# Performance work log

Hardware: AMD Instinct MI355X
Metric: run time of the kernel (lower is better)

## Reference

```python
import jax, jax.numpy as jnp
import numpy as np
import math

B, L, D, H, FF = 32, 512, 512, 8, 2048
DH = D // H
EPS = 1e-5

def pe_table(L, D):
    pos = jnp.arange(L, dtype=jnp.float32)[:, None]
    div = jnp.exp(jnp.arange(0, D, 2, dtype=jnp.float32) * (-(math.log(10000.0) / D)))
    pe = jnp.zeros((L, D), dtype=jnp.float32)
    pe = pe.at[:, 0::2].set(jnp.sin(pos * div))
    pe = pe.at[:, 1::2].set(jnp.cos(pos * div))
    return pe

def setup_inputs() -> dict:
    key = jax.random.key(0)
    ks = jax.random.split(key, 16)
    s = 0.02
    inp = {
        "x": jax.random.normal(ks[0], (B, L, D), jnp.float32),
        "mask": jnp.ones((B, L), jnp.int32),
        "speaker_emb": jax.random.normal(ks[1], (B, L, D), jnp.float32),
        "Wg": jax.random.normal(ks[2], (D, D), jnp.float32) * s,
        "Wq": jax.random.normal(ks[3], (D, D), jnp.float32) * s,
        "bq": jnp.zeros((D,), jnp.float32),
        "Wk": jax.random.normal(ks[4], (D, D), jnp.float32) * s,
        "bk": jnp.zeros((D,), jnp.float32),
        "Wv": jax.random.normal(ks[5], (D, D), jnp.float32) * s,
        "bv": jnp.zeros((D,), jnp.float32),
        "Wo": jax.random.normal(ks[6], (D, D), jnp.float32) * s,
        "bo": jnp.zeros((D,), jnp.float32),
        "ln_g": jnp.ones((D,), jnp.float32),
        "ln_b": jnp.zeros((D,), jnp.float32),
        "W1": jax.random.normal(ks[7], (FF, D), jnp.float32) * s,
        "b1": jnp.zeros((FF,), jnp.float32),
        "W2": jax.random.normal(ks[8], (D, FF), jnp.float32) * s,
        "b2": jnp.zeros((D,), jnp.float32),
    }
    return inp

def layer_norm(x, g, b):
    mu = jnp.mean(x, axis=-1, keepdims=True)
    var = jnp.var(x, axis=-1, keepdims=True)
    return (x - mu) * jax.lax.rsqrt(var + EPS) * g + b

def reference(x, mask, speaker_emb, Wg, Wq, bq, Wk, bk, Wv, bv, Wo, bo, ln_g, ln_b, W1, b1, W2, b2):
    # DynamicGating: sigmoid(x W^T) * x
    x = jax.nn.sigmoid(x @ Wg.T) * x
    # speaker embedding + sinusoidal positional encoding (dropout is eval/no-op)
    x = x + speaker_emb + pe_table(L, D)[None, :, :]
    # Multi-head self-attention (eager, full score matrix)
    q = (x @ Wq.T + bq).reshape(B, L, H, DH).transpose(0, 2, 1, 3) / math.sqrt(DH)
    k = (x @ Wk.T + bk).reshape(B, L, H, DH).transpose(0, 2, 1, 3)
    v = (x @ Wv.T + bv).reshape(B, L, H, DH).transpose(0, 2, 1, 3)
    scores = jnp.einsum("bhqd,bhkd->bhqk", q, k)  # (B,H,L,L)
    key_mask = (mask == 0)[:, None, None, :]  # mask keys where mask==0
    scores = jnp.where(key_mask, jnp.float32(-1e10), scores)
    attn = jax.nn.softmax(scores, axis=-1)
    ctx = jnp.einsum("bhqk,bhkd->bhqd", attn, v)
    ctx = ctx.transpose(0, 2, 1, 3).reshape(B, L, D)
    attn_out = ctx @ Wo.T + bo
    h = attn_out + x  # residual (dropout no-op)
    # FeedForwardNet: note GELU applied after BOTH linears (faithful to source)
    mid = jax.nn.gelu(layer_norm(h, ln_g, ln_b) @ W1.T + b1, approximate=True)
    out = jax.nn.gelu(mid @ W2.T + b2, approximate=True)
    return out + h
```

## Files before the change

kernel.cpp:

```cpp
#include <hip/hip_runtime.h>
#include <math.h>

#define Bn 32
#define Ln 512
#define Dn 512
#define Hn 8
#define DHn 64
#define FFn 2048
#define Mn (Bn*Ln)
#define QKVS 1536

typedef __attribute__((ext_vector_type(4))) float f32x4;
typedef __attribute__((ext_vector_type(8))) short short8;

__device__ __forceinline__ float bf2f(ushort u){ return __uint_as_float(((unsigned)u) << 16); }
__device__ __forceinline__ ushort f2bf(float f){
  unsigned u = __float_as_uint(f);
  u += 0x7FFFu + ((u >> 16) & 1u);
  return (ushort)(u >> 16);
}
__device__ __forceinline__ float gelu_fast(float x){
  float y2 = 1.5957691216057308f * (x + 0.044715f*x*x*x);
  return x / (1.0f + __expf(-y2));
}

__device__ __forceinline__ void gload_lds16(const ushort* g, ushort* l){
  __builtin_amdgcn_global_load_lds(
      (__attribute__((address_space(1))) void*)(void*)g,
      (__attribute__((address_space(3))) void*)(void*)l, 16, 0, 0);
}

__device__ __forceinline__ void cvt4(const float* __restrict__ in, ushort* __restrict__ out, int u){
  float4 v = *(const float4*)(in + u*4);
  ushort4 o;
  o.x = f2bf(v.x); o.y = f2bf(v.y); o.z = f2bf(v.z); o.w = f2bf(v.w);
  *(ushort4*)(out + u*4) = o;
}

__global__ __launch_bounds__(256) void prep_kernel(
    const float* __restrict__ Wg, const float* __restrict__ Wq, const float* __restrict__ Wk,
    const float* __restrict__ Wv, const float* __restrict__ Wo, const float* __restrict__ W1,
    const float* __restrict__ W2,
    const float* __restrict__ bq, const float* __restrict__ bk, const float* __restrict__ bv,
    ushort* __restrict__ wgb, ushort* __restrict__ wqkvb, ushort* __restrict__ wob,
    ushort* __restrict__ w1b, ushort* __restrict__ w2b,
    float* __restrict__ pe, float* __restrict__ bqkv)
{
  int u = blockIdx.x*256 + threadIdx.x;
  const int WU = 65536, FU = 262144;
  if (u < WU){ cvt4(Wg, wgb, u); return; }            u -= WU;
  if (u < WU){ cvt4(Wq, wqkvb, u); return; }          u -= WU;
  if (u < WU){ cvt4(Wk, wqkvb + 262144, u); return; } u -= WU;
  if (u < WU){ cvt4(Wv, wqkvb + 524288, u); return; } u -= WU;
  if (u < WU){ cvt4(Wo, wob, u); return; }            u -= WU;
  if (u < FU){ cvt4(W1, w1b, u); return; }            u -= FU;
  if (u < FU){ cvt4(W2, w2b, u); return; }            u -= FU;
  if (u < WU){
    int e = u*4; int l = e >> 9; int d0 = e & 511;
    #pragma unroll
    for (int p=0;p<2;p++){
      int i = (d0 >> 1) + p;
      float dv = expf((float)(2*i) * (-9.210340371976184f/512.0f));
      float ang = (float)l * dv;
      pe[e + 2*p]     = sinf(ang);
      pe[e + 2*p + 1] = cosf(ang);
    }
    return;
  }
  u -= WU;
  if (u < 384){
    int e = u*4;
    #pragma unroll
    for (int j=0;j<4;j++){
      int i = e + j;
      bqkv[i] = (i < 512) ? bq[i] : (i < 1024) ? bk[i-512] : bv[i-1024];
    }
  }
}

__global__ void cvt_kernel(const float* __restrict__ in, ushort* __restrict__ out, int n){
  int i = (blockIdx.x*256 + threadIdx.x)*4;
  if (i >= n) return;
  cvt4(in, out, i >> 2);
}

template<int MODE>
__global__ __launch_bounds__(512) void gemm_kernel(
    const ushort* __restrict__ A, const ushort* __restrict__ W,
    const float* __restrict__ bias,
    const float* __restrict__ res,
    const ushort* __restrict__ rbf,
    const float* __restrict__ spk, const float* __restrict__ pe,
    float* __restrict__ outf, ushort* __restrict__ outb, ushort* __restrict__ outb2,
    int K, int N, int gx)
{
  __shared__ ushort lbuf[3][24576];
  int t = threadIdx.x;
  int wave = t >> 6, lane = t & 63;
  int wrow = wave >> 2, wcol = wave & 3;
  int g = lane >> 4, r16 = lane & 15;

  int nwg = gx * (Mn/256);
  int wg = blockIdx.x;
  int tile = (wg & 7)*(nwg >> 3) + (wg >> 3);
  int trow = tile / gx;
  int tcol = tile - trow*gx;
  int rowBase = trow * 256;
  int colBase = tcol * 128;

  int srow8 = lane >> 3;
  int sucol = ((lane & 7) ^ srow8) * 8;
  const ushort* gA = A + (size_t)(rowBase + wave*8 + srow8)*K + sucol;
  const ushort* gW = W + (size_t)(colBase + wave*8 + srow8)*K + sucol;

  int NT = K >> 6;

  f32x4 acc[8][2];
  #pragma unroll
  for (int m=0;m<8;m++)
    #pragma unroll
    for (int n=0;n<2;n++) acc[m][n] = (f32x4)0.0f;

  #pragma unroll
  for (int c=0;c<4;c++) gload_lds16(gA + (size_t)c*64*K,      &lbuf[0][c*4096 + wave*512]);
  #pragma unroll
  for (int c=0;c<2;c++) gload_lds16(gW + (size_t)c*64*K,      &lbuf[0][16384 + c*4096 + wave*512]);
  #pragma unroll
  for (int c=0;c<4;c++) gload_lds16(gA + (size_t)c*64*K + 64, &lbuf[1][c*4096 + wave*512]);
  #pragma unroll
  for (int c=0;c<2;c++) gload_lds16(gW + (size_t)c*64*K + 64, &lbuf[1][16384 + c*4096 + wave*512]);
  asm volatile("s_waitcnt vmcnt(6)" ::: "memory");
  __builtin_amdgcn_s_barrier();

  int cur = 0, stg = 2;
  for (int kt = 0; kt < NT; ++kt){
    if (kt + 2 < NT){
      int k0 = (kt + 2) << 6;
      #pragma unroll
      for (int c=0;c<4;c++) gload_lds16(gA + (size_t)c*64*K + k0, &lbuf[stg][c*4096 + wave*512]);
      #pragma unroll
      for (int c=0;c<2;c++) gload_lds16(gW + (size_t)c*64*K + k0, &lbuf[stg][16384 + c*4096 + wave*512]);
    }
    const ushort* ab = &lbuf[cur][0];
    const ushort* bb = &lbuf[cur][16384];
    __builtin_amdgcn_s_setprio(1);
    #pragma unroll
    for (int ks=0; ks<2; ks++){
      short8 af[8], bfr[2];
      #pragma unroll
      for (int m=0;m<8;m++){
        int row = wrow*128 + m*16 + r16;
        af[m] = *(const short8*)&ab[row*64 + (((ks<<2)+g) ^ (row & 7))*8];
      }
      #pragma unroll
      for (int n=0;n<2;n++){
        int row = wcol*32 + n*16 + r16;
        bfr[n] = *(const short8*)&bb[row*64 + (((ks<<2)+g) ^ (row & 7))*8];
      }
      #pragma unroll
      for (int m=0;m<8;m++)
        #pragma unroll
        for (int n=0;n<2;n++)
          acc[m][n] = __builtin_amdgcn_mfma_f32_16x16x32_bf16(af[m], bfr[n], acc[m][n], 0, 0, 0);
    }
    __builtin_amdgcn_s_setprio(0);
    if (kt + 1 < NT){
      if (kt + 2 < NT) asm volatile("s_waitcnt vmcnt(6)" ::: "memory");
      else             asm volatile("s_waitcnt vmcnt(0)" ::: "memory");
      __builtin_amdgcn_s_barrier();
    }
    cur = (cur == 2) ? 0 : cur + 1;
    stg = (stg == 2) ? 0 : stg + 1;
  }

  if constexpr (MODE == 0 || MODE == 1 || MODE == 3){
    bool vpart = false;
    if constexpr (MODE == 1) vpart = (colBase >= 1024);
    if (!vpart){
      __syncthreads();
      ushort* ct = &lbuf[0][0];
      #pragma unroll
      for (int m=0;m<8;m++){
        #pragma unroll
        for (int n=0;n<2;n++){
          int col = wcol*32 + n*16 + r16;
          int gc = colBase + col;
          float sc = 1.0f;
          if constexpr (MODE == 1) sc = (gc < 512) ? 0.125f : 1.0f;
          #pragma unroll
          for (int j=0;j<4;j++){
            int row = wrow*128 + m*16 + g*4 + j;
            float c = acc[m][n][j];
            ushort val;
            if constexpr (MODE == 0){
              int gr = rowBase + row;
              size_t o = (size_t)gr * N + gc;
              float s = 1.0f/(1.0f + __expf(-c));
              val = f2bf(s * res[o] + spk[o] + pe[(gr & (Ln-1))*Dn + gc]);
            } else if constexpr (MODE == 3){
              val = f2bf(gelu_fast(c + bias[gc]));
            } else {
              val = f2bf((c + bias[gc]) * sc);
            }
            ct[row*128 + (col ^ ((row & 7) << 3))] = val;
          }
        }
      }
      __syncthreads();
      int r = t >> 1, ch = (t & 1)*64;
      ushort* dst = outb + (size_t)(rowBase + r)*N + colBase + ch;
      #pragma unroll
      for (int q=0;q<8;q++){
        int col = (ch + q*8) ^ ((r & 7) << 3);
        *(short8*)(dst + q*8) = *(const short8*)&ct[r*128 + col];
      }
    } else {
      #pragma unroll
      for (int m=0;m<8;m++){
        #pragma unroll
        for (int n=0;n<2;n++){
          int gc = colBase + wcol*32 + n*16 + r16;
          int dhg = gc - 1024;
          int gr0 = rowBase + wrow*128 + m*16 + g*4;
          int bb2 = gr0 >> 9, l0 = gr0 & 511;
          ushort4 o4;
          o4.x = f2bf(acc[m][n][0] + bias[gc]);
          o4.y = f2bf(acc[m][n][1] + bias[gc]);
          o4.z = f2bf(acc[m][n][2] + bias[gc]);
          o4.w = f2bf(acc[m][n][3] + bias[gc]);
          *(ushort4*)(outb2 + ((size_t)(bb2*Hn + (dhg>>6))*DHn + (dhg & 63))*Ln + l0) = o4;
        }
      }
    }
  } else {
    #pragma unroll
    for (int m=0;m<8;m++){
      #pragma unroll
      for (int n=0;n<2;n++){
        int gc = colBase + wcol*32 + n*16 + r16;
        #pragma unroll
        for (int j=0;j<4;j++){
          int gr = rowBase + wrow*128 + m*16 + g*4 + j;
          size_t o = (size_t)gr * N + gc;
          float c = acc[m][n][j];
          if constexpr (MODE == 2){
            outf[o] = c + bias[gc] + bf2f(rbf[o]);
          } else {
            outf[o] = gelu_fast(c + bias[gc]) + res[o];
          }
        }
      }
    }
  }
}

__global__ __launch_bounds__(256) void attn_mfma_kernel(
    const ushort* __restrict__ qb, const ushort* __restrict__ kb, const ushort* __restrict__ vtb,
    const int* __restrict__ mask, ushort* __restrict__ ctxb)
{
  __shared__ ushort lK[2][64][72];
  __shared__ ushort lVt[2][64][72];
  __shared__ ushort lP[4][32][72];

  int t = threadIdx.x;
  int w = t >> 6, lane = t & 63;
  int g = lane >> 4, r16 = lane & 15;
  int b = blockIdx.z, h = blockIdx.y;
  int qbase = blockIdx.x*128 + w*32;

  int key0 = t >> 3;
  int c8s = (t & 7) * 8;
  const ushort* kbase = kb + (size_t)(b*Ln)*QKVS + h*DHn + c8s;
  const ushort* vt = vtb + (size_t)((b*Hn + h)*DHn) * Ln;

  short8 af_q[2][2];
  #pragma unroll
  for (int m=0;m<2;m++)
    #pragma unroll
    for (int ks=0;ks<2;ks++)
      af_q[m][ks] = *(const short8*)(qb + (size_t)(b*Ln + qbase + m*16 + r16)*QKVS + h*DHn + ks*32 + g*8);

  f32x4 acc_ctx[2][4];
  #pragma unroll
  for (int m=0;m<2;m++)
    #pragma unroll
    for (int n=0;n<4;n++) acc_ctx[m][n] = (f32x4)0.0f;
  float mrun[2][4], lrun[2][4];
  #pragma unroll
  for (int m=0;m<2;m++)
    #pragma unroll
    for (int j=0;j<4;j++){ mrun[m][j] = -INFINITY; lrun[m][j] = 0.0f; }

  {
    short8 ka = *(const short8*)(kbase + (size_t)key0*QKVS);
    short8 kc = *(const short8*)(kbase + (size_t)(key0+32)*QKVS);
    short8 va = *(const short8*)(vt + (size_t)key0*Ln + c8s);
    short8 vc = *(const short8*)(vt + (size_t)(key0+32)*Ln + c8s);
    *(short8*)&lK[0][key0][c8s] = ka;
    *(short8*)&lK[0][key0+32][c8s] = kc;
    *(short8*)&lVt[0][key0][c8s] = va;
    *(short8*)&lVt[0][key0+32][c8s] = vc;
  }
  __syncthreads();
  int cb = 0;

  for (int kb0 = 0; kb0 < Ln; kb0 += 64){
    short8 kna, knb, vna, vnb;
    bool more = (kb0 + 64 < Ln);
    if (more){
      kna = *(const short8*)(kbase + (size_t)(kb0 + 64 + key0)*QKVS);
      knb = *(const short8*)(kbase + (size_t)(kb0 + 64 + key0 + 32)*QKVS);
      vna = *(const short8*)(vt + (size_t)key0*Ln + kb0 + 64 + c8s);
      vnb = *(const short8*)(vt + (size_t)(key0+32)*Ln + kb0 + 64 + c8s);
    }

    f32x4 acc_s[2][4];
    #pragma unroll
    for (int m=0;m<2;m++)
      #pragma unroll
      for (int n=0;n<4;n++) acc_s[m][n] = (f32x4)0.0f;
    __builtin_amdgcn_s_setprio(1);
    #pragma unroll
    for (int ks=0;ks<2;ks++){
      short8 bf_k[4];
      #pragma unroll
      for (int n=0;n<4;n++)
        bf_k[n] = *(const short8*)&lK[cb][n*16 + r16][ks*32 + g*8];
      #pragma unroll
      for (int m=0;m<2;m++)
        #pragma unroll
        for (int n=0;n<4;n++)
          acc_s[m][n] = __builtin_amdgcn_mfma_f32_16x16x32_bf16(af_q[m][ks], bf_k[n], acc_s[m][n], 0, 0, 0);
    }
    __builtin_amdgcn_s_setprio(0);

    #pragma unroll
    for (int n=0;n<4;n++){
      if (mask[b*Ln + kb0 + n*16 + r16] == 0){
        #pragma unroll
        for (int m=0;m<2;m++)
          #pragma unroll
          for (int j=0;j<4;j++) acc_s[m][n][j] = -1e10f;
      }
    }

    #pragma unroll
    for (int m=0;m<2;m++){
      #pragma unroll
      for (int j=0;j<4;j++){
        float tmax = fmaxf(fmaxf(acc_s[m][0][j], acc_s[m][1][j]),
                           fmaxf(acc_s[m][2][j], acc_s[m][3][j]));
        #pragma unroll
        for (int off=1; off<16; off<<=1) tmax = fmaxf(tmax, __shfl_xor(tmax, off));
        float newm = fmaxf(mrun[m][j], tmax);
        float alpha = __expf(mrun[m][j] - newm);
        float p0 = __expf(acc_s[m][0][j] - newm);
        float p1 = __expf(acc_s[m][1][j] - newm);
        float p2 = __expf(acc_s[m][2][j] - newm);
        float p3 = __expf(acc_s[m][3][j] - newm);
        float tsum = (p0+p1)+(p2+p3);
        #pragma unroll
        for (int off=1; off<16; off<<=1) tsum += __shfl_xor(tsum, off);
        lrun[m][j] = lrun[m][j]*alpha + tsum;
        mrun[m][j] = newm;
        #pragma unroll
        for (int n2=0;n2<4;n2++) acc_ctx[m][n2][j] *= alpha;
        int prow = m*16 + g*4 + j;
        lP[w][prow][0*16 + r16] = f2bf(p0);
        lP[w][prow][1*16 + r16] = f2bf(p1);
        lP[w][prow][2*16 + r16] = f2bf(p2);
        lP[w][prow][3*16 + r16] = f2bf(p3);
      }
    }

    __builtin_amdgcn_s_setprio(1);
    #pragma unroll
    for (int ks2=0;ks2<2;ks2++){
      short8 af_p[2], bf_v[4];
      #pragma unroll
      for (int m=0;m<2;m++)
        af_p[m] = *(const short8*)&lP[w][m*16 + r16][ks2*32 + g*8];
      #pragma unroll
      for (int n=0;n<4;n++)
        bf_v[n] = *(const short8*)&lVt[cb][n*16 + r16][ks2*32 + g*8];
      #pragma unroll
      for (int m=0;m<2;m++)
        #pragma unroll
        for (int n=0;n<4;n++)
          acc_ctx[m][n] = __builtin_amdgcn_mfma_f32_16x16x32_bf16(af_p[m], bf_v[n], acc_ctx[m][n], 0, 0, 0);
    }
    __builtin_amdgcn_s_setprio(0);

    if (more){
      *(short8*)&lK[cb^1][key0][c8s] = kna;
      *(short8*)&lK[cb^1][key0+32][c8s] = knb;
      *(short8*)&lVt[cb^1][key0][c8s] = vna;
      *(short8*)&lVt[cb^1][key0+32][c8s] = vnb;
    }
    __syncthreads();
    cb ^= 1;
  }

  #pragma unroll
  for (int m=0;m<2;m++){
    #pragma unroll
    for (int j=0;j<4;j++){
      float inv = 1.0f / lrun[m][j];
      int gr = qbase + m*16 + g*4 + j;
      #pragma unroll
      for (int n=0;n<4;n++){
        ctxb[(size_t)(b*Ln + gr)*Dn + h*DHn + n*16 + r16] = f2bf(acc_ctx[m][n][j] * inv);
      }
    }
  }
}

__global__ __launch_bounds__(256) void ln_kernel(
    const float* __restrict__ hbuf, const float* __restrict__ gamma, const float* __restrict__ beta,
    ushort* __restrict__ out)
{
  int row = blockIdx.x*4 + (threadIdx.x >> 6);
  int lane = threadIdx.x & 63;
  const float* p = hbuf + (size_t)row*Dn + lane*8;
  float4 a = *(const float4*)p;
  float4 c = *(const float4*)(p + 4);
  float v[8] = {a.x,a.y,a.z,a.w,c.x,c.y,c.z,c.w};
  float s = 0.f, ss = 0.f;
  #pragma unroll
  for (int j=0;j<8;j++){ s += v[j]; ss += v[j]*v[j]; }
  #pragma unroll
  for (int off=32; off>0; off>>=1){ s += __shfl_xor(s, off); ss += __shfl_xor(ss, off); }
  float mu = s * (1.0f/Dn);
  float var = ss * (1.0f/Dn) - mu*mu;
  float rstd = rsqrtf(var + 1e-5f);
  ushort o8[8];
  #pragma unroll
  for (int j=0;j<8;j++) o8[j] = f2bf((v[j]-mu)*rstd*gamma[lane*8+j] + beta[lane*8+j]);
  ushort* op = out + (size_t)row*Dn + lane*8;
  *(ushort4*)op       = make_ushort4(o8[0],o8[1],o8[2],o8[3]);
  *(ushort4*)(op + 4) = make_ushort4(o8[4],o8[5],o8[6],o8[7]);
}

extern "C" void kernel_launch(void* const* d_in, const int* in_sizes, int n_in,
                              void* d_out, int out_size, void* d_ws, size_t ws_size,
                              hipStream_t stream) {
  (void)in_sizes; (void)n_in; (void)out_size; (void)ws_size;
  const float* x    = (const float*)d_in[0];
  const int*   mask = (const int*)d_in[1];
  const float* spk  = (const float*)d_in[2];
  const float* Wg   = (const float*)d_in[3];
  const float* Wq   = (const float*)d_in[4];  const float* bq = (const float*)d_in[5];
  const float* Wk   = (const float*)d_in[6];  const float* bk = (const float*)d_in[7];
  const float* Wv   = (const float*)d_in[8];  const float* bv = (const float*)d_in[9];
  const float* Wo   = (const float*)d_in[10]; const float* bo = (const float*)d_in[11];
  const float* lng  = (const float*)d_in[12]; const float* lnbeta = (const float*)d_in[13];
  const float* W1   = (const float*)d_in[14]; const float* b1 = (const float*)d_in[15];
  const float* W2   = (const float*)d_in[16]; const float* b2 = (const float*)d_in[17];
  float* out = (float*)d_out;

  char* w = (char*)d_ws;
  size_t o = 0;
  ushort* xbf   = (ushort*)(w + o); o += (size_t)Mn*Dn*2;
  ushort* xinb  = (ushort*)(w + o); o += (size_t)Mn*Dn*2;
  ushort* qkvb  = (ushort*)(w + o); o += (size_t)Mn*QKVS*2;
  ushort* vtb   = (ushort*)(w + o); o += (size_t)Mn*Dn*2;
  ushort* ctxb  = (ushort*)(w + o); o += (size_t)Mn*Dn*2;
  float*  hbuf  = (float*)(w + o);  o += (size_t)Mn*Dn*4;
  ushort* lnbuf = (ushort*)(w + o); o += (size_t)Mn*Dn*2;
  ushort* wgb   = (ushort*)(w + o); o += (size_t)Dn*Dn*2;
  ushort* wqkvb = (ushort*)(w + o); o += (size_t)QKVS*Dn*2;
  ushort* wob   = (ushort*)(w + o); o += (size_t)Dn*Dn*2;
  ushort* w1b   = (ushort*)(w + o); o += (size_t)FFn*Dn*2;
  ushort* w2b   = (ushort*)(w + o); o += (size_t)Dn*FFn*2;
  float*  pebuf = (float*)(w + o);  o += (size_t)Ln*Dn*4;
  float*  bqkv  = (float*)(w + o);  o += (size_t)QKVS*4;
  ushort* midb  = xbf;

  hipLaunchKernelGGL(prep_kernel, dim3(3586), dim3(256), 0, stream,
                     Wg, Wq, Wk, Wv, Wo, W1, W2, bq, bk, bv,
                     wgb, wqkvb, wob, w1b, w2b, pebuf, bqkv);
  hipLaunchKernelGGL(cvt_kernel, dim3((Mn*Dn/4)/256), dim3(256), 0, stream, x, xbf, Mn*Dn);

  hipLaunchKernelGGL((gemm_kernel<0>), dim3((Dn/128)*(Mn/256)), dim3(512), 0, stream,
                     xbf, wgb, (const float*)nullptr, x, (const ushort*)nullptr, spk, pebuf,
                     (float*)nullptr, xinb, (ushort*)nullptr, Dn, Dn, Dn/128);
  hipLaunchKernelGGL((gemm_kernel<1>), dim3((QKVS/128)*(Mn/256)), dim3(512), 0, stream,
                     xinb, wqkvb, bqkv, (const float*)nullptr, (const ushort*)nullptr,
                     (const float*)nullptr, (const float*)nullptr,
                     (float*)nullptr, qkvb, vtb, Dn, QKVS, QKVS/128);
  hipLaunchKernelGGL(attn_mfma_kernel, dim3(Ln/128, Hn, Bn), dim3(256), 0, stream,
                     qkvb, qkvb + 512, vtb, mask, ctxb);
  hipLaunchKernelGGL((gemm_kernel<2>), dim3((Dn/128)*(Mn/256)), dim3(512), 0, stream,
                     ctxb, wob, bo, (const float*)nullptr, xinb, (const float*)nullptr,
                     (const float*)nullptr, hbuf, (ushort*)nullptr, (ushort*)nullptr, Dn, Dn, Dn/128);
  hipLaunchKernelGGL(ln_kernel, dim3(Mn/4), dim3(256), 0, stream, hbuf, lng, lnbeta, lnbuf);
  hipLaunchKernelGGL((gemm_kernel<3>), dim3((FFn/128)*(Mn/256)), dim3(512), 0, stream,
                     lnbuf, w1b, b1, (const float*)nullptr, (const ushort*)nullptr,
                     (const float*)nullptr, (const float*)nullptr,
                     (float*)nullptr, midb, (ushort*)nullptr, Dn, FFn, FFn/128);
  hipLaunchKernelGGL((gemm_kernel<4>), dim3((Dn/128)*(Mn/256)), dim3(512), 0, stream,
                     midb, w2b, b2, hbuf, (const ushort*)nullptr,
                     (const float*)nullptr, (const float*)nullptr,
                     out, (ushort*)nullptr, (ushort*)nullptr, FFn, Dn, Dn/128);
}
```

Baseline: 324.0 us.

## Add 256x256 GEMM for QKV/FFN1, widen attention blocks, fold x conversion into prep

Adds a new gemm256 kernel with 256x256 output tiles, double-buffered direct-to-LDS loads and an XOR-swizzled LDS layout. It is used for the QKV projection and the first FFN linear, and stages output through LDS so global stores are coalesced. The attention kernel moves to 512 threads and 256 queries per block, so each K/V tile staged in LDS serves more queries. The separate x-to-bf16 conversion launch is merged into the prep kernel. Larger tiles cut global traffic but increase register and LDS pressure and lower occupancy.

Result: faster. 303.0 us (-6.5%).

```diff
diff --git a/kernel.cpp b/kernel.cpp
--- a/kernel.cpp
+++ b/kernel.cpp
@@ -38,6 +38,7 @@
 }
 
 __global__ __launch_bounds__(256) void prep_kernel(
+    const float* __restrict__ x, ushort* __restrict__ xbf,
     const float* __restrict__ Wg, const float* __restrict__ Wq, const float* __restrict__ Wk,
     const float* __restrict__ Wv, const float* __restrict__ Wo, const float* __restrict__ W1,
     const float* __restrict__ W2,
@@ -47,7 +48,8 @@
     float* __restrict__ pe, float* __restrict__ bqkv)
 {
   int u = blockIdx.x*256 + threadIdx.x;
-  const int WU = 65536, FU = 262144;
+  const int XU = 2097152, WU = 65536, FU = 262144;
+  if (u < XU){ cvt4(x, xbf, u); return; }             u -= XU;
   if (u < WU){ cvt4(Wg, wgb, u); return; }            u -= WU;
   if (u < WU){ cvt4(Wq, wqkvb, u); return; }          u -= WU;
   if (u < WU){ cvt4(Wk, wqkvb + 262144, u); return; } u -= WU;
@@ -76,12 +78,6 @@
       bqkv[i] = (i < 512) ? bq[i] : (i < 1024) ? bk[i-512] : bv[i-1024];
     }
   }
-}
-
-__global__ void cvt_kernel(const float* __restrict__ in, ushort* __restrict__ out, int n){
-  int i = (blockIdx.x*256 + threadIdx.x)*4;
-  if (i >= n) return;
-  cvt4(in, out, i >> 2);
 }
 
 template<int MODE>
@@ -254,19 +250,144 @@
   }
 }
 
-__global__ __launch_bounds__(256) void attn_mfma_kernel(
+template<int MODE>
+__global__ __launch_bounds__(512) void gemm256_kernel(
+    const ushort* __restrict__ A, const ushort* __restrict__ W,
+    const float* __restrict__ bias,
+    ushort* __restrict__ outb, ushort* __restrict__ outb2,
+    int K, int N, int gx)
+{
+  __shared__ ushort lbuf[2][2][16384];
+  int t = threadIdx.x;
+  int wave = t >> 6, lane = t & 63;
+  int wrow = wave >> 2, wcol = wave & 3;
+  int g = lane >> 4, r16 = lane & 15;
+
+  int nwg = gx * (Mn/256);
+  int wg = blockIdx.x;
+  int tile = (wg & 7)*(nwg >> 3) + (wg >> 3);
+  int trow = tile / gx;
+  int tcol = tile - trow*gx;
+  int rowBase = trow * 256;
+  int colBase = tcol * 256;
+
+  int srow8 = lane >> 3;
+  int sucol = ((lane & 7) ^ srow8) * 8;
+  const ushort* gA = A + (size_t)(rowBase + wave*8 + srow8)*K + sucol;
+  const ushort* gW = W + (size_t)(colBase + wave*8 + srow8)*K + sucol;
+
+  f32x4 acc[8][4];
+  #pragma unroll
+  for (int m=0;m<8;m++)
+    #pragma unroll
+    for (int n=0;n<4;n++) acc[m][n] = (f32x4)0.0f;
+
+  #pragma unroll
+  for (int c=0;c<4;c++){
+    gload_lds16(gA + (size_t)c*64*K, &lbuf[0][0][c*4096 + wave*512]);
+    gload_lds16(gW + (size_t)c*64*K, &lbuf[0][1][c*4096 + wave*512]);
+  }
+
+  int cb = 0;
+  for (int k0 = 0; k0 < K; k0 += 64){
+    if (k0 + 64 < K){
+      #pragma unroll
+      for (int c=0;c<4;c++){
+        gload_lds16(gA + (size_t)c*64*K + k0 + 64, &lbuf[cb^1][0][c*4096 + wave*512]);
+        gload_lds16(gW + (size_t)c*64*K + k0 + 64, &lbuf[cb^1][1][c*4096 + wave*512]);
+      }
+      asm volatile("s_waitcnt vmcnt(8)" ::: "memory");
+    } else {
+      asm volatile("s_waitcnt vmcnt(0)" ::: "memory");
+    }
+    __builtin_amdgcn_s_barrier();
+    #pragma unroll
+    for (int ks=0; ks<2; ks++){
+      short8 af[8], bfr[4];
+      #pragma unroll
+      for (int m=0;m<8;m++){
+        int row = wrow*128 + m*16 + r16;
+        af[m] = *(const short8*)&lbuf[cb][0][row*64 + (((ks<<2)+g) ^ (r16 & 7))*8];
+      }
+      #pragma unroll
+      for (int n=0;n<4;n++){
+        int row = wcol*64 + n*16 + r16;
+        bfr[n] = *(const short8*)&lbuf[cb][1][row*64 + (((ks<<2)+g) ^ (r16 & 7))*8];
+      }
+      #pragma unroll
+      for (int m=0;m<8;m++)
+        #pragma unroll
+        for (int n=0;n<4;n++)
+          acc[m][n] = __builtin_amdgcn_mfma_f32_16x16x32_bf16(af[m], bfr[n], acc[m][n], 0, 0, 0);
+    }
+    __builtin_amdgcn_s_barrier();
+    cb ^= 1;
+  }
+
+  bool vpart = false;
+  if constexpr (MODE == 1) vpart = (colBase >= 1024);
+  if (!vpart){
+    ushort* ct = &lbuf[0][0][0];
+    #pragma unroll
+    for (int m=0;m<8;m++){
+      #pragma unroll
+      for (int n=0;n<4;n++){
+        int col = wcol*64 + n*16 + r16;
+        int gc = colBase + col;
+        float sc = 1.0f;
+        if constexpr (MODE == 1) sc = (gc < 512) ? 0.125f : 1.0f;
+        #pragma unroll
+        for (int j=0;j<4;j++){
+          int row = wrow*128 + m*16 + g*4 + j;
+          float c = acc[m][n][j];
+          ushort val;
+          if constexpr (MODE == 3) val = f2bf(gelu_fast(c + bias[gc]));
+          else                     val = f2bf((c + bias[gc]) * sc);
+          ct[row*256 + (col ^ ((row & 7) << 3))] = val;
+        }
+      }
+    }
+    __syncthreads();
+    int r = t >> 1, ch = (t & 1)*128;
+    ushort* dst = outb + (size_t)(rowBase + r)*N + colBase + ch;
+    #pragma unroll
+    for (int q=0;q<16;q++){
+      int col = (ch + q*8) ^ ((r & 7) << 3);
+      *(short8*)(dst + q*8) = *(const short8*)&ct[r*256 + col];
+    }
+  } else {
+    #pragma unroll
+    for (int m=0;m<8;m++){
+      #pragma unroll
+      for (int n=0;n<4;n++){
+        int gc = colBase + wcol*64 + n*16 + r16;
+        int dhg = gc - 1024;
+        int gr0 = rowBase + wrow*128 + m*16 + g*4;
+        int bb = gr0 >> 9, l0 = gr0 & 511;
+        ushort4 o4;
+        o4.x = f2bf(acc[m][n][0] + bias[gc]);
+        o4.y = f2bf(acc[m][n][1] + bias[gc]);
+        o4.z = f2bf(acc[m][n][2] + bias[gc]);
+        o4.w = f2bf(acc[m][n][3] + bias[gc]);
+        *(ushort4*)(outb2 + ((size_t)(bb*Hn + (dhg>>6))*DHn + (dhg & 63))*Ln + l0) = o4;
+      }
+    }
+  }
+}
+
+__global__ __launch_bounds__(512) void attn_mfma_kernel(
     const ushort* __restrict__ qb, const ushort* __restrict__ kb, const ushort* __restrict__ vtb,
     const int* __restrict__ mask, ushort* __restrict__ ctxb)
 {
   __shared__ ushort lK[2][64][72];
   __shared__ ushort lVt[2][64][72];
-  __shared__ ushort lP[4][32][72];
+  __shared__ ushort lP[8][32][72];
 
   int t = threadIdx.x;
   int w = t >> 6, lane = t & 63;
   int g = lane >> 4, r16 = lane & 15;
   int b = blockIdx.z, h = blockIdx.y;
-  int qbase = blockIdx.x*128 + w*32;
+  int qbase = blockIdx.x*256 + w*32;
 
   int key0 = t >> 3;
   int c8s = (t & 7) * 8;
@@ -293,25 +414,19 @@
 
   {
     short8 ka = *(const short8*)(kbase + (size_t)key0*QKVS);
-    short8 kc = *(const short8*)(kbase + (size_t)(key0+32)*QKVS);
     short8 va = *(const short8*)(vt + (size_t)key0*Ln + c8s);
-    short8 vc = *(const short8*)(vt + (size_t)(key0+32)*Ln + c8s);
     *(short8*)&lK[0][key0][c8s] = ka;
-    *(short8*)&lK[0][key0+32][c8s] = kc;
     *(short8*)&lVt[0][key0][c8s] = va;
-    *(short8*)&lVt[0][key0+32][c8s] = vc;
   }
   __syncthreads();
   int cb = 0;
 
   for (int kb0 = 0; kb0 < Ln; kb0 += 64){
-    short8 kna, knb, vna, vnb;
+    short8 kna, vna;
     bool more = (kb0 + 64 < Ln);
     if (more){
       kna = *(const short8*)(kbase + (size_t)(kb0 + 64 + key0)*QKVS);
-      knb = *(const short8*)(kbase + (size_t)(kb0 + 64 + key0 + 32)*QKVS);
       vna = *(const short8*)(vt + (size_t)key0*Ln + kb0 + 64 + c8s);
-      vnb = *(const short8*)(vt + (size_t)(key0+32)*Ln + kb0 + 64 + c8s);
     }
 
     f32x4 acc_s[2][4];
@@ -393,9 +508,7 @@
 
     if (more){
       *(short8*)&lK[cb^1][key0][c8s] = kna;
-      *(short8*)&lK[cb^1][key0+32][c8s] = knb;
       *(short8*)&lVt[cb^1][key0][c8s] = vna;
-      *(short8*)&lVt[cb^1][key0+32][c8s] = vnb;
     }
     __syncthreads();
     cb ^= 1;
@@ -476,28 +589,23 @@
   float*  bqkv  = (float*)(w + o);  o += (size_t)QKVS*4;
   ushort* midb  = xbf;
 
-  hipLaunchKernelGGL(prep_kernel, dim3(3586), dim3(256), 0, stream,
-                     Wg, Wq, Wk, Wv, Wo, W1, W2, bq, bk, bv,
+  hipLaunchKernelGGL(prep_kernel, dim3(11778), dim3(256), 0, stream,
+                     x, xbf, Wg, Wq, Wk, Wv, Wo, W1, W2, bq, bk, bv,
                      wgb, wqkvb, wob, w1b, w2b, pebuf, bqkv);
-  hipLaunchKernelGGL(cvt_kernel, dim3((Mn*Dn/4)/256), dim3(256), 0, stream, x, xbf, Mn*Dn);
 
   hipLaunchKernelGGL((gemm_kernel<0>), dim3((Dn/128)*(Mn/256)), dim3(512), 0, stream,
                      xbf, wgb, (const float*)nullptr, x, (const ushort*)nullptr, spk, pebuf,
                      (float*)nullptr, xinb, (ushort*)nullptr, Dn, Dn, Dn/128);
-  hipLaunchKernelGGL((gemm_kernel<1>), dim3((QKVS/128)*(Mn/256)), dim3(512), 0, stream,
-                     xinb, wqkvb, bqkv, (const float*)nullptr, (const ushort*)nullptr,
-                     (const float*)nullptr, (const float*)nullptr,
-                     (float*)nullptr, qkvb, vtb, Dn, QKVS, QKVS/128);
-  hipLaunchKernelGGL(attn_mfma_kernel, dim3(Ln/128, Hn, Bn), dim3(256), 0, stream,
+  hipLaunchKernelGGL((gemm256_kernel<1>), dim3((QKVS/256)*(Mn/256)), dim3(512), 0, stream,
+                     xinb, wqkvb, bqkv, qkvb, vtb, Dn, QKVS, QKVS/256);
+  hipLaunchKernelGGL(attn_mfma_kernel, dim3(Ln/256, Hn, Bn), dim3(512), 0, stream,
                      qkvb, qkvb + 512, vtb, mask, ctxb);
   hipLaunchKernelGGL((gemm_kernel<2>), dim3((Dn/128)*(Mn/256)), dim3(512), 0, stream,
                      ctxb, wob, bo, (const float*)nullptr, xinb, (const float*)nullptr,
                      (const float*)nullptr, hbuf, (ushort*)nullptr, (ushort*)nullptr, Dn, Dn, Dn/128);
   hipLaunchKernelGGL(ln_kernel, dim3(Mn/4), dim3(256), 0, stream, hbuf, lng, lnbeta, lnbuf);
-  hipLaunchKernelGGL((gemm_kernel<3>), dim3((FFn/128)*(Mn/256)), dim3(512), 0, stream,
-                     lnbuf, w1b, b1, (const float*)nullptr, (const ushort*)nullptr,
-                     (const float*)nullptr, (const float*)nullptr,
-                     (float*)nullptr, midb, (ushort*)nullptr, Dn, FFn, FFn/128);
+  hipLaunchKernelGGL((gemm256_kernel<3>), dim3((FFn/256)*(Mn/256)), dim3(512), 0, stream,
+                     lnbuf, w1b, b1, midb, (ushort*)nullptr, Dn, FFn, FFn/256);
   hipLaunchKernelGGL((gemm_kernel<4>), dim3((Dn/128)*(Mn/256)), dim3(512), 0, stream,
                      midb, w2b, b2, hbuf, (const ushort*)nullptr,
                      (const float*)nullptr, (const float*)nullptr,
```
